# Kernel optimization log

Hardware: AMD Instinct MI355X
Metric: run time of the kernel (lower is better)

The kernel has to match this reference:

```python
import jax, jax.numpy as jnp
import numpy as np

BN_EPS = 1e-5

def setup_inputs() -> dict:
    key = jax.random.key(0)
    ks = jax.random.split(key, 6)
    N, C, T, V = 64, 64, 300, 25
    Ci, Co, S = 16, 64, 3  # inter_channels = out//4, num_subset = 3
    x = jax.random.normal(ks[0], (N, C, T, V), dtype=jnp.float32)
    # static (non-trainable) adjacency buffer; graph_attn is init.constant_(1)
    A_static = jax.random.uniform(ks[1], (S, V, V), dtype=jnp.float32)
    graph_attn = jnp.ones((S, V, V), jnp.float32)
    # stacked 1x1 conv weights for the 3 subsets: (S, out_c, in_c)
    Wg = jax.random.normal(ks[2], (S, Co, C), jnp.float32) * 0.05
    bg = jnp.zeros((S, Co), jnp.float32)
    Wa = jax.random.normal(ks[3], (S, Ci, C), jnp.float32) * 0.05
    ba = jnp.zeros((S, Ci), jnp.float32)
    Wb = jax.random.normal(ks[4], (S, Ci, C), jnp.float32) * 0.05
    bb = jnp.zeros((S, Ci), jnp.float32)
    # BatchNorm2d (eval mode: running stats)
    gamma = jnp.ones((Co,), jnp.float32)
    beta = jnp.zeros((Co,), jnp.float32)
    run_mean = jnp.zeros((Co,), jnp.float32)
    run_var = jnp.ones((Co,), jnp.float32)
    return {"x": x, "A_static": A_static, "graph_attn": graph_attn,
            "Wg": Wg, "bg": bg, "Wa": Wa, "ba": ba, "Wb": Wb, "bb": bb,
            "gamma": gamma, "beta": beta, "run_mean": run_mean, "run_var": run_var}

def _conv1x1(x, W, b):
    # x: (N,C,T,V), W: (O,C), b: (O,) -> (N,O,T,V)
    return jnp.einsum('nctv,oc->notv', x, W) + b[None, :, None, None]

def reference(x, A_static, graph_attn, Wg, bg, Wa, ba, Wb, bb, gamma, beta, run_mean, run_var):
    N, C, T, V = x.shape
    Ci = Wa.shape[1]
    A = A_static + graph_attn            # (3, V, V)
    x_flat = x.reshape(N, C * T, V)
    hidden = jnp.zeros((), x.dtype)
    for i in range(Wg.shape[0]):
        a = _conv1x1(x, Wa[i], ba[i])                                  # (N,Ci,T,V)
        b2 = _conv1x1(x, Wb[i], bb[i])                                 # (N,Ci,T,V)
        A1 = a.transpose(0, 3, 1, 2).reshape(N, V, Ci * T)             # (N,V,Ci*T)
        A2 = b2.reshape(N, Ci * T, V)                                  # (N,Ci*T,V)
        attn = jax.nn.softmax(jnp.matmul(A1, A2) / (Ci * T), axis=-2)  # softmax over dim -2
        attn = attn + A[i]                                             # (N,V,V)
        y = jnp.matmul(x_flat, attn).reshape(N, C, T, V)
        hidden = hidden + _conv1x1(y, Wg[i], bg[i])
    inv = (gamma / jnp.sqrt(run_var + BN_EPS))[None, :, None, None]
    hn = (hidden - run_mean[None, :, None, None]) * inv + beta[None, :, None, None]
    return jax.nn.relu(hn + x)  # in_channels == out_channels -> identity residual
```

## Files before the change

kernel.cpp:

```cpp
#include <hip/hip_runtime.h>

typedef unsigned short u16;
typedef __attribute__((ext_vector_type(8))) short short8;
typedef __attribute__((ext_vector_type(4))) unsigned short ushort4v;
typedef __attribute__((ext_vector_type(4))) float float4v;

#define NB 64
#define CB 64
#define TB 300
#define VB 25
#define TVB 7500
#define CTVB 480000

static __device__ __forceinline__ float bf2f(u16 a) {
    union { unsigned u; float f; } x; x.u = ((unsigned)a) << 16; return x.f;
}
static __device__ __forceinline__ u16 f2bf(float f) {
    union { float f; unsigned u; } x; x.f = f;
    unsigned r = x.u + 0x7fffu + ((x.u >> 16) & 1u);
    return (u16)(r >> 16);
}

__global__ __launch_bounds__(256) void kA(
    const float* __restrict__ xg, const float* __restrict__ Wa, const float* __restrict__ ba,
    const float* __restrict__ Wb, const float* __restrict__ bb, float* __restrict__ Sws)
{
    __shared__ u16 xT[4][32][72];
    __shared__ u16 asT[3][32][72];
    __shared__ u16 bsT[3][32][72];
    const int tid  = threadIdx.x;
    const int lane = tid & 63;
    const int w    = tid >> 6;
    const int l15  = lane & 15;
    const int q    = lane >> 4;
    const int n    = blockIdx.y;
    const int t0   = blockIdx.x * 20;

    for (int e = tid; e < 4 * 7 * 72; e += 256) {
        int tt = e / (7 * 72);
        int r  = e - tt * (7 * 72);
        xT[tt][25 + r / 72][r % 72] = 0;
    }

    short8 waf[2], wbf[2];
    float ba_r[4], bb_r[4];
    if (w < 3) {
        const float* wap = Wa + w * 1024;
        const float* wbp = Wb + w * 1024;
        #pragma unroll
        for (int kf = 0; kf < 2; ++kf) {
            short8 fa, fb;
            int base = l15 * 64 + kf * 32 + q * 8;
            #pragma unroll
            for (int j = 0; j < 8; ++j) {
                fa[j] = (short)f2bf(wap[base + j]);
                fb[j] = (short)f2bf(wbp[base + j]);
            }
            waf[kf] = fa; wbf[kf] = fb;
        }
        #pragma unroll
        for (int r = 0; r < 4; ++r) {
            ba_r[r] = ba[w * 16 + q * 4 + r];
            bb_r[r] = bb[w * 16 + q * 4 + r];
        }
    }

    float4v accS[3];
    #pragma unroll
    for (int i = 0; i < 3; ++i) accS[i] = (float4v){0.f, 0.f, 0.f, 0.f};

    const float* xb = xg + (size_t)n * CTVB;

    for (int g = 0; g < 5; ++g) {
        __syncthreads();
        for (int e = tid; e < 6400; e += 256) {
            int c = e / 100;
            int j = e - c * 100;
            int tt = j / 25;
            int u  = j - tt * 25;
            xT[tt][u][c] = f2bf(xb[c * TVB + (t0 + g * 4) * 25 + j]);
        }
        __syncthreads();
        if (w < 3) {
            #pragma unroll
            for (int tt = 0; tt < 4; ++tt) {
                float4v aA0 = {0,0,0,0}, aA1 = {0,0,0,0}, aB0 = {0,0,0,0}, aB1 = {0,0,0,0};
                #pragma unroll
                for (int kf = 0; kf < 2; ++kf) {
                    short8 x0 = *(const short8*)&xT[tt][l15][kf * 32 + q * 8];
                    short8 x1 = *(const short8*)&xT[tt][16 + l15][kf * 32 + q * 8];
                    aA0 = __builtin_amdgcn_mfma_f32_16x16x32_bf16(waf[kf], x0, aA0, 0, 0, 0);
                    aA1 = __builtin_amdgcn_mfma_f32_16x16x32_bf16(waf[kf], x1, aA1, 0, 0, 0);
                    aB0 = __builtin_amdgcn_mfma_f32_16x16x32_bf16(wbf[kf], x0, aB0, 0, 0, 0);
                    aB1 = __builtin_amdgcn_mfma_f32_16x16x32_bf16(wbf[kf], x1, aB1, 0, 0, 0);
                }
                ushort4v pa0, pa1, pb0, pb1;
                #pragma unroll
                for (int r = 0; r < 4; ++r) {
                    pa0[r] = f2bf(aA0[r] + ba_r[r]);
                    pa1[r] = f2bf(aA1[r] + ba_r[r]);
                    pb0[r] = f2bf(aB0[r] + bb_r[r]);
                    pb1[r] = f2bf(aB1[r] + bb_r[r]);
                }
                int kb = tt * 16 + q * 4;
                *(ushort4v*)&asT[w][l15][kb]      = pa0;
                *(ushort4v*)&asT[w][16 + l15][kb] = pa1;
                *(ushort4v*)&bsT[w][l15][kb]      = pb0;
                *(ushort4v*)&bsT[w][16 + l15][kb] = pb1;
            }
        }
        __syncthreads();
        const int mt = w >> 1, nt = w & 1;
        #pragma unroll
        for (int i = 0; i < 3; ++i) {
            #pragma unroll
            for (int ks = 0; ks < 2; ++ks) {
                short8 af  = *(const short8*)&asT[i][mt * 16 + l15][ks * 32 + q * 8];
                short8 bf_ = *(const short8*)&bsT[i][nt * 16 + l15][ks * 32 + q * 8];
                accS[i] = __builtin_amdgcn_mfma_f32_16x16x32_bf16(af, bf_, accS[i], 0, 0, 0);
            }
        }
    }
    const int mt = w >> 1, nt = w & 1;
    #pragma unroll
    for (int i = 0; i < 3; ++i) {
        #pragma unroll
        for (int r = 0; r < 4; ++r) {
            int u = mt * 16 + q * 4 + r;
            int v = nt * 16 + l15;
            if (u < 25 && v < 25)
                atomicAdd(&Sws[(i * 64 + n) * 625 + u * 25 + v], accS[i][r]);
        }
    }
}

__global__ __launch_bounds__(64) void kS(float* __restrict__ Sws,
    const float* __restrict__ Ast, const float* __restrict__ Gat)
{
    int g = blockIdx.x;
    int i = g >> 6;
    int v = threadIdx.x;
    if (v >= 25) return;
    float vals[25];
    float m = -1e30f;
    #pragma unroll
    for (int u = 0; u < 25; ++u) {
        float s = Sws[g * 625 + u * 25 + v] * (1.0f / 4800.0f);
        vals[u] = s;
        m = fmaxf(m, s);
    }
    float sum = 0.f;
    #pragma unroll
    for (int u = 0; u < 25; ++u) { float e = __expf(vals[u] - m); vals[u] = e; sum += e; }
    float isum = 1.f / sum;
    #pragma unroll
    for (int u = 0; u < 25; ++u) {
        int idx = i * 625 + u * 25 + v;
        Sws[g * 625 + u * 25 + v] = vals[u] * isum + Ast[idx] + Gat[idx];
    }
}

__global__ __launch_bounds__(256) void kB(
    const float* __restrict__ xg, const float* __restrict__ Wgp, const float* __restrict__ bgp,
    const float* __restrict__ gam, const float* __restrict__ bet, const float* __restrict__ rmu,
    const float* __restrict__ rva, const float* __restrict__ attnw, float* __restrict__ outg)
{
    __shared__ u16 xsu[6][64][32];
    __shared__ u16 ysT[32][200];
    __shared__ u16 pTs[3][32][40];
    const int tid  = threadIdx.x;
    const int lane = tid & 63;
    const int w    = tid >> 6;
    const int l15  = lane & 15;
    const int q    = lane >> 4;
    const int n    = blockIdx.y;
    const int t0   = blockIdx.x * 6;

    for (int e = tid; e < 3 * 32 * 40; e += 256) ((u16*)pTs)[e] = 0;
    const float* xb = xg + (size_t)n * CTVB;
    for (int e = tid; e < 64 * 150; e += 256) {
        int c = e / 150;
        int j = e - c * 150;
        int tt = j / 25;
        int u  = j - tt * 25;
        xsu[tt][c][u] = f2bf(xb[c * TVB + t0 * 25 + j]);
    }
    for (int e = tid; e < 6 * 64 * 7; e += 256) {
        int tt = e / (64 * 7);
        int r  = e - tt * (64 * 7);
        xsu[tt][r / 7][25 + r % 7] = 0;
    }
    __syncthreads();
    for (int e = tid; e < 1875; e += 256) {
        int i = e / 625;
        int r = e - i * 625;
        int u = r / 25;
        int v = r - u * 25;
        pTs[i][v][u] = f2bf(attnw[(i * 64 + n) * 625 + r]);
    }
    short8 wgf[6];
    const int o_row = w * 16 + l15;
    #pragma unroll
    for (int kf = 0; kf < 6; ++kf) {
        int i  = kf >> 1;
        int c0 = (kf & 1) * 32 + q * 8;
        const float* p = Wgp + i * 4096 + o_row * 64 + c0;
        short8 f;
        #pragma unroll
        for (int j = 0; j < 8; ++j) f[j] = (short)f2bf(p[j]);
        wgf[kf] = f;
    }
    float invr[4], add0r[4];
    #pragma unroll
    for (int r = 0; r < 4; ++r) {
        int o = w * 16 + q * 4 + r;
        float gv = gam[o], bt = bet[o], mu = rmu[o], vv = rva[o];
        float bgs = bgp[o] + bgp[64 + o] + bgp[128 + o];
        float iv = gv * rsqrtf(vv + 1e-5f);
        invr[r] = iv;
        add0r[r] = (bgs - mu) * iv + bt;
    }
    __syncthreads();
    short8 pf[3][2];
    #pragma unroll
    for (int i = 0; i < 3; ++i)
        #pragma unroll
        for (int nt = 0; nt < 2; ++nt)
            pf[i][nt] = *(const short8*)&pTs[i][nt * 16 + l15][q * 8];

    for (int tl = 0; tl < 6; ++tl) {
        short8 xf = *(const short8*)&xsu[tl][w * 16 + l15][q * 8];
        #pragma unroll
        for (int i = 0; i < 3; ++i) {
            #pragma unroll
            for (int nt = 0; nt < 2; ++nt) {
                float4v acc = {0, 0, 0, 0};
                acc = __builtin_amdgcn_mfma_f32_16x16x32_bf16(xf, pf[i][nt], acc, 0, 0, 0);
                ushort4v pk;
                #pragma unroll
                for (int r = 0; r < 4; ++r) pk[r] = f2bf(acc[r]);
                *(ushort4v*)&ysT[nt * 16 + l15][i * 64 + w * 16 + q * 4] = pk;
            }
        }
        __syncthreads();
        #pragma unroll
        for (int nt = 0; nt < 2; ++nt) {
            float4v acc = {0, 0, 0, 0};
            #pragma unroll
            for (int kf = 0; kf < 6; ++kf) {
                short8 yf = *(const short8*)&ysT[nt * 16 + l15][kf * 32 + q * 8];
                acc = __builtin_amdgcn_mfma_f32_16x16x32_bf16(wgf[kf], yf, acc, 0, 0, 0);
            }
            int v = nt * 16 + l15;
            if (v < 25) {
                size_t ob = (size_t)n * CTVB + (size_t)(t0 + tl) * 25 + v;
                #pragma unroll
                for (int r = 0; r < 4; ++r) {
                    int o = w * 16 + q * 4 + r;
                    float xres = bf2f(xsu[tl][o][v]);
                    float val = fmaf(acc[r], invr[r], add0r[r]) + xres;
                    val = fmaxf(val, 0.f);
                    outg[ob + (size_t)o * TVB] = val;
                }
            }
        }
        __syncthreads();
    }
}

extern "C" void kernel_launch(void* const* d_in, const int* in_sizes, int n_in,
                              void* d_out, int out_size, void* d_ws, size_t ws_size,
                              hipStream_t stream) {
    const float* x    = (const float*)d_in[0];
    const float* Ast  = (const float*)d_in[1];
    const float* Gat  = (const float*)d_in[2];
    const float* Wg   = (const float*)d_in[3];
    const float* bg   = (const float*)d_in[4];
    const float* Wa   = (const float*)d_in[5];
    const float* ba   = (const float*)d_in[6];
    const float* Wb   = (const float*)d_in[7];
    const float* bb   = (const float*)d_in[8];
    const float* gam  = (const float*)d_in[9];
    const float* bet  = (const float*)d_in[10];
    const float* rmu  = (const float*)d_in[11];
    const float* rva  = (const float*)d_in[12];
    float* out = (float*)d_out;
    float* Sws = (float*)d_ws;

    hipMemsetAsync(Sws, 0, 192 * 625 * sizeof(float), stream);
    kA<<<dim3(15, 64), 256, 0, stream>>>(x, Wa, ba, Wb, bb, Sws);
    kS<<<dim3(192), 64, 0, stream>>>(Sws, Ast, Gat);
    kB<<<dim3(50, 64), 256, 0, stream>>>(x, Wg, bg, gam, bet, rmu, rva, Sws, out);
}
```

Measured before the change: 362.8 us.

## Shrink per-block time tiles, vectorize loads, cheaper bf16 packing, fp32 residual

Both kernels now take smaller time tiles per block (kA 12 steps, kB 3 steps), so the grids grow to 25x64 and 100x64 and launch bounds add occupancy hints. Global x loads become float2 and the weight loads float4. bf16 conversion switches to round-half-up with perm-based pair packing. kB now reads the residual in fp32 from global memory instead of the bf16 shared copy, and one __syncthreads is removed. The changes target load and conversion overhead and aim for better latency hiding, at the cost of more atomics in kA, more redundant per-block setup, and a slightly different rounding mode.

Result: slower. 410.9 us (+13.2%).

```diff
diff --git a/kernel.cpp b/kernel.cpp
--- a/kernel.cpp
+++ b/kernel.cpp
@@ -2,26 +2,23 @@
 
 typedef unsigned short u16;
 typedef __attribute__((ext_vector_type(8))) short short8;
-typedef __attribute__((ext_vector_type(4))) unsigned short ushort4v;
 typedef __attribute__((ext_vector_type(4))) float float4v;
 
-#define NB 64
-#define CB 64
-#define TB 300
-#define VB 25
 #define TVB 7500
 #define CTVB 480000
 
-static __device__ __forceinline__ float bf2f(u16 a) {
-    union { unsigned u; float f; } x; x.u = ((unsigned)a) << 16; return x.f;
-}
-static __device__ __forceinline__ u16 f2bf(float f) {
+union U8S { short8 s; uint4 u; };
+
+static __device__ __forceinline__ u16 f2bfc(float f) {
     union { float f; unsigned u; } x; x.f = f;
-    unsigned r = x.u + 0x7fffu + ((x.u >> 16) & 1u);
-    return (u16)(r >> 16);
-}
-
-__global__ __launch_bounds__(256) void kA(
+    return (u16)((x.u + 0x8000u) >> 16);
+}
+static __device__ __forceinline__ unsigned pk2(float a, float b) {
+    union { float f; unsigned u; } xa, xb; xa.f = a; xb.f = b;
+    return __builtin_amdgcn_perm(xb.u + 0x8000u, xa.u + 0x8000u, 0x07060302u);
+}
+
+__global__ __launch_bounds__(256, 3) void kA(
     const float* __restrict__ xg, const float* __restrict__ Wa, const float* __restrict__ ba,
     const float* __restrict__ Wb, const float* __restrict__ bb, float* __restrict__ Sws)
 {
@@ -34,29 +31,27 @@
     const int l15  = lane & 15;
     const int q    = lane >> 4;
     const int n    = blockIdx.y;
-    const int t0   = blockIdx.x * 20;
+    const int t0   = blockIdx.x * 12;
 
     for (int e = tid; e < 4 * 7 * 72; e += 256) {
-        int tt = e / (7 * 72);
-        int r  = e - tt * (7 * 72);
+        int tt = e / 504;
+        int r  = e - tt * 504;
         xT[tt][25 + r / 72][r % 72] = 0;
     }
 
     short8 waf[2], wbf[2];
     float ba_r[4], bb_r[4];
     if (w < 3) {
-        const float* wap = Wa + w * 1024;
-        const float* wbp = Wb + w * 1024;
         #pragma unroll
         for (int kf = 0; kf < 2; ++kf) {
-            short8 fa, fb;
-            int base = l15 * 64 + kf * 32 + q * 8;
-            #pragma unroll
-            for (int j = 0; j < 8; ++j) {
-                fa[j] = (short)f2bf(wap[base + j]);
-                fb[j] = (short)f2bf(wbp[base + j]);
-            }
-            waf[kf] = fa; wbf[kf] = fb;
+            const float* pa = Wa + w * 1024 + l15 * 64 + kf * 32 + q * 8;
+            const float* pb = Wb + w * 1024 + l15 * 64 + kf * 32 + q * 8;
+            float4 a0 = *(const float4*)pa, a1 = *(const float4*)(pa + 4);
+            float4 b0 = *(const float4*)pb, b1 = *(const float4*)(pb + 4);
+            U8S ta, tb;
+            ta.u = make_uint4(pk2(a0.x, a0.y), pk2(a0.z, a0.w), pk2(a1.x, a1.y), pk2(a1.z, a1.w));
+            tb.u = make_uint4(pk2(b0.x, b0.y), pk2(b0.z, b0.w), pk2(b1.x, b1.y), pk2(b1.z, b1.w));
+            waf[kf] = ta.s; wbf[kf] = tb.s;
         }
         #pragma unroll
         for (int r = 0; r < 4; ++r) {
@@ -71,14 +66,20 @@
 
     const float* xb = xg + (size_t)n * CTVB;
 
-    for (int g = 0; g < 5; ++g) {
-        __syncthreads();
-        for (int e = tid; e < 6400; e += 256) {
-            int c = e / 100;
-            int j = e - c * 100;
-            int tt = j / 25;
-            int u  = j - tt * 25;
-            xT[tt][u][c] = f2bf(xb[c * TVB + (t0 + g * 4) * 25 + j]);
+    for (int g = 0; g < 3; ++g) {
+        __syncthreads();
+        const float* xs = xb + (t0 + g * 4) * 25;
+        #pragma unroll 2
+        for (int e = tid; e < 3200; e += 256) {
+            int c = e / 50;
+            int p = e - c * 50;
+            int j = 2 * p;
+            float2 v2 = *(const float2*)(xs + c * TVB + j);
+            int tt0 = j / 25, u0 = j - tt0 * 25;
+            int j1 = j + 1;
+            int tt1 = j1 / 25, u1 = j1 - tt1 * 25;
+            xT[tt0][u0][c] = f2bfc(v2.x);
+            xT[tt1][u1][c] = f2bfc(v2.y);
         }
         __syncthreads();
         if (w < 3) {
@@ -94,19 +95,15 @@
                     aB0 = __builtin_amdgcn_mfma_f32_16x16x32_bf16(wbf[kf], x0, aB0, 0, 0, 0);
                     aB1 = __builtin_amdgcn_mfma_f32_16x16x32_bf16(wbf[kf], x1, aB1, 0, 0, 0);
                 }
-                ushort4v pa0, pa1, pb0, pb1;
-                #pragma unroll
-                for (int r = 0; r < 4; ++r) {
-                    pa0[r] = f2bf(aA0[r] + ba_r[r]);
-                    pa1[r] = f2bf(aA1[r] + ba_r[r]);
-                    pb0[r] = f2bf(aB0[r] + bb_r[r]);
-                    pb1[r] = f2bf(aB1[r] + bb_r[r]);
-                }
                 int kb = tt * 16 + q * 4;
-                *(ushort4v*)&asT[w][l15][kb]      = pa0;
-                *(ushort4v*)&asT[w][16 + l15][kb] = pa1;
-                *(ushort4v*)&bsT[w][l15][kb]      = pb0;
-                *(ushort4v*)&bsT[w][16 + l15][kb] = pb1;
+                uint2 ua0 = { pk2(aA0[0] + ba_r[0], aA0[1] + ba_r[1]), pk2(aA0[2] + ba_r[2], aA0[3] + ba_r[3]) };
+                uint2 ua1 = { pk2(aA1[0] + ba_r[0], aA1[1] + ba_r[1]), pk2(aA1[2] + ba_r[2], aA1[3] + ba_r[3]) };
+                uint2 ub0 = { pk2(aB0[0] + bb_r[0], aB0[1] + bb_r[1]), pk2(aB0[2] + bb_r[2], aB0[3] + bb_r[3]) };
+                uint2 ub1 = { pk2(aB1[0] + bb_r[0], aB1[1] + bb_r[1]), pk2(aB1[2] + bb_r[2], aB1[3] + bb_r[3]) };
+                *(uint2*)&asT[w][l15][kb]      = ua0;
+                *(uint2*)&asT[w][16 + l15][kb] = ua1;
+                *(uint2*)&bsT[w][l15][kb]      = ub0;
+                *(uint2*)&bsT[w][16 + l15][kb] = ub1;
             }
         }
         __syncthreads();
@@ -160,12 +157,12 @@
     }
 }
 
-__global__ __launch_bounds__(256) void kB(
+__global__ __launch_bounds__(256, 4) void kB(
     const float* __restrict__ xg, const float* __restrict__ Wgp, const float* __restrict__ bgp,
     const float* __restrict__ gam, const float* __restrict__ bet, const float* __restrict__ rmu,
     const float* __restrict__ rva, const float* __restrict__ attnw, float* __restrict__ outg)
 {
-    __shared__ u16 xsu[6][64][32];
+    __shared__ u16 xsu[3][64][32];
     __shared__ u16 ysT[32][200];
     __shared__ u16 pTs[3][32][40];
     const int tid  = threadIdx.x;
@@ -174,41 +171,50 @@
     const int l15  = lane & 15;
     const int q    = lane >> 4;
     const int n    = blockIdx.y;
-    const int t0   = blockIdx.x * 6;
+    const int t0   = blockIdx.x * 3;
 
     for (int e = tid; e < 3 * 32 * 40; e += 256) ((u16*)pTs)[e] = 0;
     const float* xb = xg + (size_t)n * CTVB;
-    for (int e = tid; e < 64 * 150; e += 256) {
-        int c = e / 150;
-        int j = e - c * 150;
-        int tt = j / 25;
-        int u  = j - tt * 25;
-        xsu[tt][c][u] = f2bf(xb[c * TVB + t0 * 25 + j]);
-    }
-    for (int e = tid; e < 6 * 64 * 7; e += 256) {
-        int tt = e / (64 * 7);
-        int r  = e - tt * (64 * 7);
+    #pragma unroll 2
+    for (int e = tid; e < 64 * 38; e += 256) {
+        int c = e / 38;
+        int p = e - c * 38;
+        const float* src = xb + c * TVB + t0 * 25;
+        if (p < 37) {
+            int j = 2 * p;
+            float2 v2 = *(const float2*)(src + j);
+            int tt0 = j / 25, u0 = j - tt0 * 25;
+            int j1 = j + 1;
+            int tt1 = j1 / 25, u1 = j1 - tt1 * 25;
+            xsu[tt0][c][u0] = f2bfc(v2.x);
+            xsu[tt1][c][u1] = f2bfc(v2.y);
+        } else {
+            xsu[2][c][24] = f2bfc(src[74]);
+        }
+    }
+    for (int e = tid; e < 3 * 64 * 7; e += 256) {
+        int tt = e / 448;
+        int r  = e - tt * 448;
         xsu[tt][r / 7][25 + r % 7] = 0;
     }
-    __syncthreads();
     for (int e = tid; e < 1875; e += 256) {
         int i = e / 625;
         int r = e - i * 625;
         int u = r / 25;
         int v = r - u * 25;
-        pTs[i][v][u] = f2bf(attnw[(i * 64 + n) * 625 + r]);
-    }
+        pTs[i][v][u] = f2bfc(attnw[(i * 64 + n) * 625 + r]);
+    }
+
     short8 wgf[6];
-    const int o_row = w * 16 + l15;
     #pragma unroll
     for (int kf = 0; kf < 6; ++kf) {
         int i  = kf >> 1;
         int c0 = (kf & 1) * 32 + q * 8;
-        const float* p = Wgp + i * 4096 + o_row * 64 + c0;
-        short8 f;
-        #pragma unroll
-        for (int j = 0; j < 8; ++j) f[j] = (short)f2bf(p[j]);
-        wgf[kf] = f;
+        const float* p = Wgp + i * 4096 + (w * 16 + l15) * 64 + c0;
+        float4 f0 = *(const float4*)p, f1 = *(const float4*)(p + 4);
+        U8S t;
+        t.u = make_uint4(pk2(f0.x, f0.y), pk2(f0.z, f0.w), pk2(f1.x, f1.y), pk2(f1.z, f1.w));
+        wgf[kf] = t.s;
     }
     float invr[4], add0r[4];
     #pragma unroll
@@ -228,7 +234,8 @@
         for (int nt = 0; nt < 2; ++nt)
             pf[i][nt] = *(const short8*)&pTs[i][nt * 16 + l15][q * 8];
 
-    for (int tl = 0; tl < 6; ++tl) {
+    #pragma unroll
+    for (int tl = 0; tl < 3; ++tl) {
         short8 xf = *(const short8*)&xsu[tl][w * 16 + l15][q * 8];
         #pragma unroll
         for (int i = 0; i < 3; ++i) {
@@ -236,10 +243,8 @@
             for (int nt = 0; nt < 2; ++nt) {
                 float4v acc = {0, 0, 0, 0};
                 acc = __builtin_amdgcn_mfma_f32_16x16x32_bf16(xf, pf[i][nt], acc, 0, 0, 0);
-                ushort4v pk;
-                #pragma unroll
-                for (int r = 0; r < 4; ++r) pk[r] = f2bf(acc[r]);
-                *(ushort4v*)&ysT[nt * 16 + l15][i * 64 + w * 16 + q * 4] = pk;
+                uint2 pk = { pk2(acc[0], acc[1]), pk2(acc[2], acc[3]) };
+                *(uint2*)&ysT[nt * 16 + l15][i * 64 + w * 16 + q * 4] = pk;
             }
         }
         __syncthreads();
@@ -253,14 +258,14 @@
             }
             int v = nt * 16 + l15;
             if (v < 25) {
-                size_t ob = (size_t)n * CTVB + (size_t)(t0 + tl) * 25 + v;
+                int base_o = w * 16 + q * 4;
+                const float* xrp = xb + (size_t)base_o * TVB + (t0 + tl) * 25 + v;
+                float* op = outg + (size_t)n * CTVB + (size_t)base_o * TVB + (t0 + tl) * 25 + v;
                 #pragma unroll
                 for (int r = 0; r < 4; ++r) {
-                    int o = w * 16 + q * 4 + r;
-                    float xres = bf2f(xsu[tl][o][v]);
+                    float xres = xrp[(size_t)r * TVB];
                     float val = fmaf(acc[r], invr[r], add0r[r]) + xres;
-                    val = fmaxf(val, 0.f);
-                    outg[ob + (size_t)o * TVB] = val;
+                    op[(size_t)r * TVB] = fmaxf(val, 0.f);
                 }
             }
         }
@@ -288,7 +293,7 @@
     float* Sws = (float*)d_ws;
 
     hipMemsetAsync(Sws, 0, 192 * 625 * sizeof(float), stream);
-    kA<<<dim3(15, 64), 256, 0, stream>>>(x, Wa, ba, Wb, bb, Sws);
+    kA<<<dim3(25, 64), 256, 0, stream>>>(x, Wa, ba, Wb, bb, Sws);
     kS<<<dim3(192), 64, 0, stream>>>(Sws, Ast, Gat);
-    kB<<<dim3(50, 64), 256, 0, stream>>>(x, Wg, bg, gam, bet, rmu, rva, Sws, out);
-}
+    kB<<<dim3(100, 64), 256, 0, stream>>>(x, Wg, bg, gam, bet, rmu, rva, Sws, out);
+}
```
